# Performance work log

Hardware: AMD Instinct MI355X
Metric: run time of the kernel (lower is better)

Reference implementation:

```python
import jax, jax.numpy as jnp
import numpy as np

CUTOFF = 8.0  # SMEAMConfig.cutoff


def _natural_cubic_coeffs(t, y):
    """Natural cubic spline coefficients. t: [K] knots, y: [K, 1] values.
    Returns per-interval (a, b, c, d), each [K-1, 1]."""
    h = t[1:] - t[:-1]                              # [K-1]
    dy = (y[1:] - y[:-1]) / h[:, None]              # [K-1, 1]
    rhs = 6.0 * (dy[1:] - dy[:-1])                  # [K-2, 1]
    main = 2.0 * (h[:-1] + h[1:])
    A = jnp.diag(main) + jnp.diag(h[1:-1], 1) + jnp.diag(h[1:-1], -1)
    m_int = jnp.linalg.solve(A, rhs)                # interior second derivatives
    z = jnp.zeros((1, y.shape[1]), dtype=y.dtype)
    M = jnp.concatenate([z, m_int, z], axis=0)      # natural BC: M0 = M_{K-1} = 0
    a = y[:-1]
    b = dy - h[:, None] * (2.0 * M[:-1] + M[1:]) / 6.0
    c = M[:-1] / 2.0
    d = (M[1:] - M[:-1]) / (6.0 * h[:, None])
    return a, b, c, d


def _spline_eval(t, coeffs, x):
    """Evaluate spline at x: [T] -> [T, 1]. Edge intervals extrapolate."""
    a, b, c, d = coeffs
    idx = jnp.clip(jnp.searchsorted(t, x, side='right') - 1, 0, t.shape[0] - 2)
    s = (x - t[idx])[:, None]
    return a[idx] + s * (b[idx] + s * (c[idx] + s * d[idx]))


def setup_inputs() -> dict:
    key = jax.random.key(0)
    N, deg, K = 10000, 32, 7
    E = N * deg
    k1, k2, k3, k4 = jax.random.split(key, 4)
    # edge displacement vectors; scaled so bond lengths fall inside [0, cutoff]
    r = jax.random.normal(k1, (E, 3), dtype=jnp.float32) * 2.0
    f_coeffs = jax.random.uniform(k2, (K, 1), dtype=jnp.float32)
    g_coeffs = jax.random.uniform(k3, (K, 1), dtype=jnp.float32)
    src = jax.random.randint(k4, (E,), 0, N, dtype=jnp.int32)
    # fixed in-degree layout: edges with destination j are indices [j*deg, (j+1)*deg)
    dst = jnp.repeat(jnp.arange(N, dtype=jnp.int32), deg)
    return {"r": r, "f_coeffs": f_coeffs, "g_coeffs": g_coeffs,
            "src": src, "dst": dst, "deg": deg}


def reference(r, f_coeffs, g_coeffs, src, dst, deg):
    E = r.shape[0]
    K = f_coeffs.shape[0]
    knots_radial = jnp.linspace(0.0, CUTOFF, K, dtype=r.dtype)
    knots_angular = jnp.linspace(-1.0, 1.0, K, dtype=r.dtype)
    f_c = _natural_cubic_coeffs(knots_radial, f_coeffs)
    g_c = _natural_cubic_coeffs(knots_angular, g_coeffs)

    # line-graph (non-backtracking) triplets: e1 ends where e2 starts
    e2 = jnp.repeat(jnp.arange(E, dtype=jnp.int32), deg)                    # [T]
    e1 = (src[:, None] * deg + jnp.arange(deg, dtype=jnp.int32)).ravel()    # [T]
    valid = src[e1] != dst[e2]   # exclude backtracking e2 = reverse(e1)

    r1 = -r[e1]                  # [T, 3]
    r2 = r[e2]                   # [T, 3]
    l1 = jnp.linalg.norm(r1, axis=1)
    l2 = jnp.linalg.norm(r2, axis=1)
    bond_cosine = jnp.clip(jnp.sum(r1 * r2, axis=1) / (l1 * l2), -1.0, 1.0)

    m = (_spline_eval(knots_radial, f_c, l1)
         * _spline_eval(knots_radial, f_c, l2)
         * _spline_eval(knots_angular, g_c, bond_cosine))    # [T, 1]
    m = jnp.where(valid[:, None], m, jnp.zeros((), dtype=m.dtype))

    # scatter-sum triplet messages onto destination edges (line-graph nodes)
    ft = jax.ops.segment_sum(m, e2, num_segments=E)           # [E, 1]
    return ft
```

## Files before the change

kernel.cpp:

```cpp
#include <hip/hip_runtime.h>
#include <hip/hip_fp16.h>

#define DEG 32
#define K_KNOTS 7
#define NINT 6

typedef _Float16 half_t;
typedef _Float16 h2 __attribute__((ext_vector_type(2)));

union UF8 {
    uint2 u;
    struct { h2 xy; h2 zf; } h;
};

__device__ inline float fdot2(h2 a, h2 b, float c) {
#if __has_builtin(__builtin_amdgcn_fdot2)
    return __builtin_amdgcn_fdot2(a, b, c, false);
#else
    return (float)a.x * (float)b.x + (float)a.y * (float)b.y + c;
#endif
}

__device__ inline void spline_coeffs(const float* __restrict__ y, float h, float4* C) {
    float dy[NINT];
#pragma unroll
    for (int i = 0; i < NINT; ++i) dy[i] = (y[i + 1] - y[i]) / h;
    float rhs[5];
#pragma unroll
    for (int i = 0; i < 5; ++i) rhs[i] = 6.0f * (dy[i + 1] - dy[i]);
    float cp[5], dp[5];
    float denom = 4.0f * h;
    cp[0] = h / denom;
    dp[0] = rhs[0] / denom;
#pragma unroll
    for (int i = 1; i < 5; ++i) {
        denom = 4.0f * h - h * cp[i - 1];
        cp[i] = h / denom;
        dp[i] = (rhs[i] - h * dp[i - 1]) / denom;
    }
    float M[K_KNOTS];
    M[0] = 0.0f; M[6] = 0.0f;
    M[5] = dp[4];
#pragma unroll
    for (int i = 3; i >= 0; --i) M[i + 1] = dp[i] - cp[i] * M[i + 2];
#pragma unroll
    for (int i = 0; i < NINT; ++i) {
        C[i].x = y[i];
        C[i].y = dy[i] - h * (2.0f * M[i] + M[i + 1]) * (1.0f / 6.0f);
        C[i].z = M[i] * 0.5f;
        C[i].w = (M[i + 1] - M[i]) / (6.0f * h);
    }
}

__global__ __launch_bounds__(256) void edge_kernel(
    const float* __restrict__ r, const float* __restrict__ fc,
    uint2* __restrict__ uf, int E) {
    __shared__ float4 sF[NINT];
    if (threadIdx.x == 0) {
        float4 c[NINT];
        spline_coeffs(fc, 8.0f / 6.0f, c);
#pragma unroll
        for (int i = 0; i < NINT; ++i) sF[i] = c[i];
    }
    __syncthreads();
    int e = blockIdx.x * blockDim.x + threadIdx.x;
    if (e >= E) return;
    float x = r[3 * e + 0];
    float y = r[3 * e + 1];
    float z = r[3 * e + 2];
    float d = x * x + y * y + z * z;
    float rl = rsqrtf(d);
    float l = d * rl;
    float u = l * (6.0f / 8.0f);
    int idx = (int)u;
    idx = idx < 0 ? 0 : (idx > NINT - 1 ? NINT - 1 : idx);
    float s = l - (8.0f / 6.0f) * (float)idx;
    float4 c = sF[idx];
    float f = c.x + s * (c.y + s * (c.z + s * c.w));
    UF8 q;
    q.h.xy.x = (half_t)(x * rl);
    q.h.xy.y = (half_t)(y * rl);
    q.h.zf.x = (half_t)(z * rl);
    q.h.zf.y = (half_t)f;
    uf[e] = q.u;
}

__global__ __launch_bounds__(256) void triplet_kernel(
    const uint2* __restrict__ uf, const float* __restrict__ gc,
    const int* __restrict__ src, const int* __restrict__ dst,
    float* __restrict__ out, int E) {
    __shared__ float4 sG[NINT];
    if (threadIdx.x == 0) {
        float4 c[NINT];
        spline_coeffs(gc, 2.0f / 6.0f, c);
#pragma unroll
        for (int i = 0; i < NINT; ++i) sG[i] = c[i];
    }
    __syncthreads();

    int t = blockIdx.x * blockDim.x + threadIdx.x;
    int e = t >> 2;
    int q = t & 3;
    if (e >= E) return;

    int a = src[e];
    int de = dst[e];
    UF8 qe; qe.u = uf[e];
    uint2 neg = qe.u;
    neg.x ^= 0x80008000u;
    neg.y ^= 0x00008000u;
    h2 ne_xy = __builtin_bit_cast(h2, neg.x);
    h2 ne_zf = __builtin_bit_cast(h2, neg.y);
    h2 ne_z0; ne_z0.x = ne_zf.x; ne_z0.y = (half_t)0.0f;
    float fe = (float)qe.h.zf.y;

    const uint4* blk = (const uint4*)(uf + (size_t)a * DEG);
    const int4* sblk = (const int4*)(src + (size_t)a * DEG);
    uint4 rq[4];
    int4 sq[2];
#pragma unroll
    for (int it = 0; it < 4; ++it) rq[it] = blk[q * 4 + it];
#pragma unroll
    for (int it = 0; it < 2; ++it) sq[it] = sblk[q * 2 + it];

    float acc = 0.0f;
#pragma unroll
    for (int rr = 0; rr < 8; ++rr) {
        uint4 qq = rq[rr >> 1];
        unsigned w0 = (rr & 1) ? qq.z : qq.x;
        unsigned w1 = (rr & 1) ? qq.w : qq.y;
        int4 sv = sq[rr >> 2];
        int s2 = (rr & 3) == 0 ? sv.x : (rr & 3) == 1 ? sv.y
               : (rr & 3) == 2 ? sv.z : sv.w;
        h2 kxy = __builtin_bit_cast(h2, w0);
        h2 kzf = __builtin_bit_cast(h2, w1);
        float cosv = fdot2(kxy, ne_xy, fdot2(kzf, ne_z0, 0.0f));
        cosv = fminf(fmaxf(cosv, -1.0f), 1.0f);
        float u = (cosv + 1.0f) * 3.0f;
        int idx = (int)u;
        idx = idx > NINT - 1 ? NINT - 1 : idx;
        float s = cosv - (-1.0f + (2.0f / 6.0f) * (float)idx);
        float4 c = sG[idx];
        float g = c.x + s * (c.y + s * (c.z + s * c.w));
        float fk = (float)kzf.y;
        float term = (s2 != de) ? fk * g : 0.0f;
        acc += term;
    }

    acc += __shfl_xor(acc, 1, 64);
    acc += __shfl_xor(acc, 2, 64);
    if (q == 0) out[e] = fe * acc;
}

extern "C" void kernel_launch(void* const* d_in, const int* in_sizes, int n_in,
                              void* d_out, int out_size, void* d_ws, size_t ws_size,
                              hipStream_t stream) {
    const float* r   = (const float*)d_in[0];
    const float* fc  = (const float*)d_in[1];
    const float* gc  = (const float*)d_in[2];
    const int* src   = (const int*)d_in[3];
    const int* dst   = (const int*)d_in[4];
    float* out = (float*)d_out;
    int E = in_sizes[3];

    uint2* uf = (uint2*)d_ws;

    int threads = 256;
    int blocks1 = (E + threads - 1) / threads;
    edge_kernel<<<blocks1, threads, 0, stream>>>(r, fc, uf, E);

    long long T2 = (long long)E * 4;
    int blocks2 = (int)((T2 + threads - 1) / threads);
    triplet_kernel<<<blocks2, threads, 0, stream>>>(uf, gc, src, dst, out, E);
}
```

Measured before the change: 81.98 us.

## Bucket edges by source node and process triplets per node with one wave

The edge kernel now also bins each edge into a per-source-node list, using an atomic counter per node with a fixed capacity of 96 slots. A new node kernel assigns one 64-lane wave per node. Each lane keeps one of the node's 32 incoming edges in registers while the wave walks the bucketed edges two at a time and reduces each edge's sum with wave shuffles. This avoids reloading each node's 32-edge block once per outgoing edge. The cost is an extra zeroing kernel, global atomics, serial dependent gathers per node, load imbalance from uneven out-degree, and silently dropped edges if a node's out-degree exceeds the capacity.

```diff
diff --git a/kernel.cpp b/kernel.cpp
--- a/kernel.cpp
+++ b/kernel.cpp
@@ -4,6 +4,7 @@
 #define DEG 32
 #define K_KNOTS 7
 #define NINT 6
+#define CAP 96
 
 typedef _Float16 half_t;
 typedef _Float16 h2 __attribute__((ext_vector_type(2)));
@@ -52,9 +53,16 @@
     }
 }
 
+__global__ __launch_bounds__(256) void zero_cnt(int* __restrict__ cnt, int N) {
+    int i = blockIdx.x * blockDim.x + threadIdx.x;
+    if (i < N) cnt[i] = 0;
+}
+
 __global__ __launch_bounds__(256) void edge_kernel(
     const float* __restrict__ r, const float* __restrict__ fc,
-    uint2* __restrict__ uf, int E) {
+    const int* __restrict__ src,
+    uint2* __restrict__ uf, int* __restrict__ cnt, int* __restrict__ perm,
+    int E) {
     __shared__ float4 sF[NINT];
     if (threadIdx.x == 0) {
         float4 c[NINT];
@@ -83,12 +91,17 @@
     q.h.zf.x = (half_t)(z * rl);
     q.h.zf.y = (half_t)f;
     uf[e] = q.u;
+
+    int a = src[e];
+    int rank = atomicAdd(&cnt[a], 1);
+    if (rank < CAP) perm[a * CAP + rank] = e;
 }
 
-__global__ __launch_bounds__(256) void triplet_kernel(
+__global__ __launch_bounds__(256) void node_kernel(
     const uint2* __restrict__ uf, const float* __restrict__ gc,
     const int* __restrict__ src, const int* __restrict__ dst,
-    float* __restrict__ out, int E) {
+    const int* __restrict__ cnt, const int* __restrict__ perm,
+    float* __restrict__ out, int N) {
     __shared__ float4 sG[NINT];
     if (threadIdx.x == 0) {
         float4 c[NINT];
@@ -98,43 +111,37 @@
     }
     __syncthreads();
 
-    int t = blockIdx.x * blockDim.x + threadIdx.x;
-    int e = t >> 2;
-    int q = t & 3;
-    if (e >= E) return;
+    int a = (blockIdx.x * blockDim.x + threadIdx.x) >> 6;
+    int lane = threadIdx.x & 63;
+    if (a >= N) return;
 
-    int a = src[e];
-    int de = dst[e];
-    UF8 qe; qe.u = uf[e];
-    uint2 neg = qe.u;
-    neg.x ^= 0x80008000u;
-    neg.y ^= 0x00008000u;
-    h2 ne_xy = __builtin_bit_cast(h2, neg.x);
-    h2 ne_zf = __builtin_bit_cast(h2, neg.y);
-    h2 ne_z0; ne_z0.x = ne_zf.x; ne_z0.y = (half_t)0.0f;
-    float fe = (float)qe.h.zf.y;
+    int j = lane & 31;
+    int half = lane >> 5;
 
-    const uint4* blk = (const uint4*)(uf + (size_t)a * DEG);
-    const int4* sblk = (const int4*)(src + (size_t)a * DEG);
-    uint4 rq[4];
-    int4 sq[2];
-#pragma unroll
-    for (int it = 0; it < 4; ++it) rq[it] = blk[q * 4 + it];
-#pragma unroll
-    for (int it = 0; it < 2; ++it) sq[it] = sblk[q * 2 + it];
+    UF8 nk; nk.u = uf[(size_t)a * DEG + j];
+    int sj = src[(size_t)a * DEG + j];
+    h2 kxy = nk.h.xy;
+    h2 kz0; kz0.x = nk.h.zf.x; kz0.y = (half_t)0.0f;
+    float fj = (float)nk.h.zf.y;
 
-    float acc = 0.0f;
-#pragma unroll
-    for (int rr = 0; rr < 8; ++rr) {
-        uint4 qq = rq[rr >> 1];
-        unsigned w0 = (rr & 1) ? qq.z : qq.x;
-        unsigned w1 = (rr & 1) ? qq.w : qq.y;
-        int4 sv = sq[rr >> 2];
-        int s2 = (rr & 3) == 0 ? sv.x : (rr & 3) == 1 ? sv.y
-               : (rr & 3) == 2 ? sv.z : sv.w;
-        h2 kxy = __builtin_bit_cast(h2, w0);
-        h2 kzf = __builtin_bit_cast(h2, w1);
-        float cosv = fdot2(kxy, ne_xy, fdot2(kzf, ne_z0, 0.0f));
+    int m = cnt[a];
+    m = m > CAP ? CAP : m;
+
+    for (int base = 0; base < m; base += 2) {
+        int mm = base + half;
+        bool live = mm < m;
+        int e = 0;
+        if (live) e = perm[a * CAP + mm];
+        UF8 qe; qe.u = uf[e];
+        int de = dst[e];
+        uint2 neg = qe.u;
+        neg.x ^= 0x80008000u;
+        neg.y ^= 0x00008000u;
+        h2 ne_xy = __builtin_bit_cast(h2, neg.x);
+        h2 ne_zf = __builtin_bit_cast(h2, neg.y);
+        float fe = (float)qe.h.zf.y;
+
+        float cosv = fdot2(kxy, ne_xy, fdot2(kz0, ne_zf, 0.0f));
         cosv = fminf(fmaxf(cosv, -1.0f), 1.0f);
         float u = (cosv + 1.0f) * 3.0f;
         int idx = (int)u;
@@ -142,14 +149,15 @@
         float s = cosv - (-1.0f + (2.0f / 6.0f) * (float)idx);
         float4 c = sG[idx];
         float g = c.x + s * (c.y + s * (c.z + s * c.w));
-        float fk = (float)kzf.y;
-        float term = (s2 != de) ? fk * g : 0.0f;
-        acc += term;
+
+        float term = (live && (sj != de)) ? fj * g : 0.0f;
+        term += __shfl_xor(term, 1, 64);
+        term += __shfl_xor(term, 2, 64);
+        term += __shfl_xor(term, 4, 64);
+        term += __shfl_xor(term, 8, 64);
+        term += __shfl_xor(term, 16, 64);
+        if (live && j == 0) out[e] = fe * term;
     }
-
-    acc += __shfl_xor(acc, 1, 64);
-    acc += __shfl_xor(acc, 2, 64);
-    if (q == 0) out[e] = fe * acc;
 }
 
 extern "C" void kernel_launch(void* const* d_in, const int* in_sizes, int n_in,
@@ -162,14 +170,18 @@
     const int* dst   = (const int*)d_in[4];
     float* out = (float*)d_out;
     int E = in_sizes[3];
+    int N = E / DEG;
 
     uint2* uf = (uint2*)d_ws;
+    int* cnt  = (int*)((char*)d_ws + (size_t)E * 8);
+    int* perm = cnt + N;
 
     int threads = 256;
-    int blocks1 = (E + threads - 1) / threads;
-    edge_kernel<<<blocks1, threads, 0, stream>>>(r, fc, uf, E);
-
-    long long T2 = (long long)E * 4;
+    zero_cnt<<<(N + threads - 1) / threads, threads, 0, stream>>>(cnt, N);
+    edge_kernel<<<(E + threads - 1) / threads, threads, 0, stream>>>(
+        r, fc, src, uf, cnt, perm, E);
+    long long T2 = (long long)N * 64;
     int blocks2 = (int)((T2 + threads - 1) / threads);
-    triplet_kernel<<<blocks2, threads, 0, stream>>>(uf, gc, src, dst, out, E);
+    node_kernel<<<blocks2, threads, 0, stream>>>(
+        uf, gc, src, dst, cnt, perm, out, N);
 }
```

Result: slower. 126.3 us (+54.1%).
